# Kernel optimization log

Hardware: AMD Instinct MI355X
Metric: run time of the kernel (lower is better)

The kernel has to match this reference:

```python
import jax, jax.numpy as jnp
import numpy as np

N_USERS = 80000
N_ITEMS = 40000
N_NODES = N_USERS + N_ITEMS
EMBED_DIM = 128
N_LAYERS = 3
N_EDGES = 1600000
BATCH = 4096


def setup_inputs() -> dict:
    key = jax.random.key(0)
    k = jax.random.split(key, 7)
    # Xavier-uniform-ish embeddings
    bound_u = float(np.sqrt(6.0 / (N_USERS + EMBED_DIM)))
    bound_i = float(np.sqrt(6.0 / (N_ITEMS + EMBED_DIM)))
    user_emb = jax.random.uniform(k[0], (N_USERS, EMBED_DIM), jnp.float32, -bound_u, bound_u)
    item_emb = jax.random.uniform(k[1], (N_ITEMS, EMBED_DIM), jnp.float32, -bound_i, bound_i)
    edge_rows = jax.random.randint(k[2], (N_EDGES,), 0, N_NODES, dtype=jnp.int32)
    edge_cols = jax.random.randint(k[3], (N_EDGES,), 0, N_NODES, dtype=jnp.int32)
    # normalized adjacency values (positive, small) standing in for D^-1/2 A D^-1/2
    edge_vals = jax.random.uniform(k[4], (N_EDGES,), jnp.float32, 0.0, 0.1)
    users = jax.random.randint(k[5], (BATCH,), 0, N_USERS, dtype=jnp.int32)
    items = jax.random.randint(k[6], (BATCH,), 0, N_ITEMS, dtype=jnp.int32)
    return {"user_emb": user_emb, "item_emb": item_emb,
            "edge_rows": edge_rows, "edge_cols": edge_cols, "edge_vals": edge_vals,
            "users": users, "items": items}


def _spmm(edge_rows, edge_cols, edge_vals, x):
    # out[r] += vals[e] * x[cols[e]]  for each edge e with rows[e]==r
    msgs = edge_vals[:, None] * x[edge_cols]          # [E, D]
    return jax.ops.segment_sum(msgs, edge_rows, num_segments=N_NODES)


def reference(user_emb, item_emb, edge_rows, edge_cols, edge_vals, users, items):
    all_emb = jnp.concatenate([user_emb, item_emb], axis=0)  # [N, D]
    acc = all_emb
    x = all_emb
    for _ in range(N_LAYERS):
        x = _spmm(edge_rows, edge_cols, edge_vals, x)
        acc = acc + x
    final = acc / jnp.asarray(N_LAYERS + 1, dtype=acc.dtype)  # mean over stacked layers
    user_all, item_all = final[:N_USERS], final[N_USERS:]
    return user_all[users], item_all[items]
```

## Files before the change

### kernel.cpp

```cpp
#include <hip/hip_runtime.h>

#define N_USERS 80000
#define N_ITEMS 40000
#define N_NODES 120000
#define DIM 128
#define N_EDGES 1600000
#define BATCH 4096

#define RPB 512
#define NB  ((N_NODES + RPB - 1) / RPB)
#define BCAP 8192
#define CHUNK 2048
#define NCHUNK ((N_EDGES + CHUNK - 1) / CHUNK)

#define INITX_BLOCKS (N_NODES * 16 / 256)
#define GATHI_BLOCKS (2 * BATCH * 32 / 256)
#define SAMP_BLOCKS  (2 * BATCH / 256)
#define KSAMP 8

__device__ __forceinline__ float bf_lo(unsigned u) { return __uint_as_float(u << 16); }
__device__ __forceinline__ float bf_hi(unsigned u) { return __uint_as_float(u & 0xFFFF0000u); }
__device__ __forceinline__ unsigned pack_bf2(float a, float b) {
    unsigned ua = __float_as_uint(a);
    ua = (ua + 0x7FFFu + ((ua >> 16) & 1u)) >> 16;
    unsigned ub = __float_as_uint(b);
    ub = (ub + 0x7FFFu + ((ub >> 16) & 1u)) & 0xFFFF0000u;
    return ua | ub;
}

__global__ void partition_prep_kernel(const int* __restrict__ rows,
                                      const int* __restrict__ cols,
                                      const float* __restrict__ vals,
                                      const float* __restrict__ ue,
                                      const float* __restrict__ ie,
                                      const int* __restrict__ users,
                                      const int* __restrict__ items,
                                      int* __restrict__ bucket_cursor,
                                      int2* __restrict__ temp,
                                      uint4* __restrict__ xb,
                                      float4* __restrict__ out,
                                      int* __restrict__ scnt,
                                      int* __restrict__ sidx) {
    __shared__ int cnt[256];
    __shared__ int sc[256];
    __shared__ int loff[256];
    __shared__ int gbase[256];
    __shared__ int lcur[256];
    __shared__ int2 stage[CHUNK];
    __shared__ unsigned char sbkt[CHUNK];

    int tid = threadIdx.x;
    int bid = blockIdx.x;

    if (bid < NCHUNK) {
        int base = bid * CHUNK;
        int nloc = min(CHUNK, N_EDGES - base);

        cnt[tid] = 0;
        __syncthreads();

        int my_r[CHUNK / 256];
        int my_c[CHUNK / 256];
        float my_v[CHUNK / 256];
        for (int k = 0; k < CHUNK / 256; ++k) {
            int i = tid + k * 256;
            if (i < nloc) {
                int e = base + i;
                int r = rows[e];
                my_r[k] = r;
                my_c[k] = cols[e];
                my_v[k] = vals[e];
                atomicAdd(&cnt[r >> 9], 1);
            }
        }
        __syncthreads();

        sc[tid] = cnt[tid];
        __syncthreads();
        for (int off = 1; off < 256; off <<= 1) {
            int t = (tid >= off) ? sc[tid - off] : 0;
            __syncthreads();
            sc[tid] += t;
            __syncthreads();
        }
        loff[tid] = sc[tid] - cnt[tid];
        if (tid < NB && cnt[tid] > 0)
            gbase[tid] = tid * BCAP + atomicAdd(&bucket_cursor[tid], cnt[tid]);
        lcur[tid] = 0;
        __syncthreads();

        for (int k = 0; k < CHUNK / 256; ++k) {
            int i = tid + k * 256;
            if (i < nloc) {
                int b = my_r[k] >> 9;
                int rank = atomicAdd(&lcur[b], 1);
                int s = loff[b] + rank;
                stage[s] = make_int2(((my_r[k] & (RPB - 1)) << 17) | my_c[k],
                                     __float_as_int(my_v[k]));
                sbkt[s] = (unsigned char)b;
            }
        }
        __syncthreads();

        for (int k = 0; k < CHUNK / 256; ++k) {
            int s = tid + k * 256;
            if (s < nloc) {
                int b = sbkt[s];
                temp[gbase[b] + (s - loff[b])] = stage[s];
            }
        }
    } else if (bid < NCHUNK + INITX_BLOCKS) {
        int t = (bid - NCHUNK) * 256 + tid;
        int n = t >> 4;
        int c = t & 15;
        const float* src = (n < N_USERS) ? (ue + (size_t)n * DIM)
                                         : (ie + (size_t)(n - N_USERS) * DIM);
        float4 a = ((const float4*)src)[c * 2];
        float4 b = ((const float4*)src)[c * 2 + 1];
        uint4 o;
        o.x = pack_bf2(a.x, a.y);
        o.y = pack_bf2(a.z, a.w);
        o.z = pack_bf2(b.x, b.y);
        o.w = pack_bf2(b.z, b.w);
        xb[t] = o;
    } else if (bid < NCHUNK + INITX_BLOCKS + GATHI_BLOCKS) {
        int t = (bid - NCHUNK - INITX_BLOCKS) * 256 + tid;
        int half = t >> 17;
        int i = t & (BATCH * 32 - 1);
        int b = i >> 5;
        int c = i & 31;
        float4 v;
        if (half == 0) {
            int u = users[b];
            v = ((const float4*)(ue + (size_t)u * DIM))[c];
        } else {
            int it = items[b];
            v = ((const float4*)(ie + (size_t)it * DIM))[c];
        }
        out[t] = v;
    } else {
        int idx = (bid - NCHUNK - INITX_BLOCKS - GATHI_BLOCKS) * 256 + tid;
        if (idx < 2 * BATCH) {
            int node = (idx < BATCH) ? users[idx] : (N_USERS + items[idx - BATCH]);
            int slot = atomicAdd(&scnt[node], 1);
            if (slot < KSAMP) sidx[node * KSAMP + slot] = idx;
        }
    }
}

__global__ void bucket_sort_kernel(const int* __restrict__ bucket_cursor,
                                   const int2* __restrict__ temp,
                                   int2* __restrict__ ep,
                                   int* __restrict__ row_beg,
                                   int* __restrict__ row_end) {
    __shared__ int rcnt[RPB];
    __shared__ int rsc[RPB];
    __shared__ int rcur[RPB];
    int tid = threadIdx.x;
    int b = blockIdx.x;
    int beg = b * BCAP;
    int end = beg + bucket_cursor[b];

    if (tid < RPB) rcnt[tid] = 0;
    __syncthreads();
    for (int i = beg + tid; i < end; i += 1024) {
        int lr = temp[i].x >> 17;
        atomicAdd(&rcnt[lr], 1);
    }
    __syncthreads();

    int v = (tid < RPB) ? rcnt[tid] : 0;
    if (tid < RPB) rsc[tid] = v;
    __syncthreads();
    for (int off = 1; off < RPB; off <<= 1) {
        int t = (tid >= off && tid < RPB) ? rsc[tid - off] : 0;
        __syncthreads();
        if (tid < RPB) rsc[tid] += t;
        __syncthreads();
    }
    if (tid < RPB) {
        int excl = rsc[tid] - v;
        int row = (b << 9) + tid;
        if (row < N_NODES) {
            row_beg[row] = beg + excl;
            row_end[row] = beg + excl + v;
        }
        rcur[tid] = excl;
    }
    __syncthreads();

    for (int i = beg + tid; i < end; i += 1024) {
        int2 t = temp[i];
        int lr = t.x >> 17;
        int col = t.x & 0x1FFFF;
        int rank = atomicAdd(&rcur[lr], 1);
        ep[beg + rank] = make_int2(col, t.y);
    }
}

#define FMA8(V, M)                                                           \
    {                                                                        \
        acc[0] += (V) * bf_lo((M).x); acc[1] += (V) * bf_hi((M).x);          \
        acc[2] += (V) * bf_lo((M).y); acc[3] += (V) * bf_hi((M).y);          \
        acc[4] += (V) * bf_lo((M).z); acc[5] += (V) * bf_hi((M).z);          \
        acc[6] += (V) * bf_lo((M).w); acc[7] += (V) * bf_hi((M).w);          \
    }

#define ROW_ACC_LOOP(BEG, END)                                               \
    int j = (BEG);                                                           \
    for (; j + 8 <= (END); j += 8) {                                         \
        int2 e[8];                                                           \
        uint4 m[8];                                                          \
        _Pragma("unroll")                                                    \
        for (int k = 0; k < 8; ++k) e[k] = ep[j + k];                        \
        _Pragma("unroll")                                                    \
        for (int k = 0; k < 8; ++k) m[k] = xb[(size_t)e[k].x * 16 + c];      \
        _Pragma("unroll")                                                    \
        for (int k = 0; k < 8; ++k) {                                        \
            float v = __int_as_float(e[k].y);                                \
            FMA8(v, m[k]);                                                   \
        }                                                                    \
    }                                                                        \
    for (; j + 2 <= (END); j += 2) {                                         \
        int2 e0 = ep[j];                                                     \
        int2 e1 = ep[j + 1];                                                 \
        uint4 m0 = xb[(size_t)e0.x * 16 + c];                                \
        uint4 m1 = xb[(size_t)e1.x * 16 + c];                                \
        float v0 = __int_as_float(e0.y);                                     \
        float v1 = __int_as_float(e1.y);                                     \
        FMA8(v0, m0);                                                        \
        FMA8(v1, m1);                                                        \
    }                                                                        \
    if (j < (END)) {                                                         \
        int2 e0 = ep[j];                                                     \
        uint4 m0 = xb[(size_t)e0.x * 16 + c];                                \
        float v0 = __int_as_float(e0.y);                                     \
        FMA8(v0, m0);                                                        \
    }

__global__ void spmm_csr_bf16_kernel(const int* __restrict__ row_beg,
                                     const int* __restrict__ row_end,
                                     const int2* __restrict__ ep,
                                     const uint4* __restrict__ xb,
                                     uint4* __restrict__ yb,
                                     const int* __restrict__ scnt,
                                     const int* __restrict__ sidx,
                                     float4* __restrict__ out) {
    int t = blockIdx.x * blockDim.x + threadIdx.x;
    int r = t >> 4;
    int c = t & 15;
    if (r >= N_NODES) return;
    float acc[8] = {0.f, 0.f, 0.f, 0.f, 0.f, 0.f, 0.f, 0.f};
    { ROW_ACC_LOOP(row_beg[r], row_end[r]) }

    uint4 o;
    o.x = pack_bf2(acc[0], acc[1]);
    o.y = pack_bf2(acc[2], acc[3]);
    o.z = pack_bf2(acc[4], acc[5]);
    o.w = pack_bf2(acc[6], acc[7]);
    yb[(size_t)r * 16 + c] = o;

    int cnt = scnt[r];
    if (cnt > 0) {
        if (cnt > KSAMP) cnt = KSAMP;
        for (int k = 0; k < cnt; ++k) {
            int slot = sidx[r * KSAMP + k];
            float4* op = out + ((size_t)slot * 32 + c * 2);
            float4 o0 = op[0];
            float4 o1 = op[1];
            o0.x += acc[0]; o0.y += acc[1]; o0.z += acc[2]; o0.w += acc[3];
            o1.x += acc[4]; o1.y += acc[5]; o1.z += acc[6]; o1.w += acc[7];
            op[0] = o0;
            op[1] = o1;
        }
    }
}

__global__ void spmm_out_kernel(const int* __restrict__ row_beg,
                                const int* __restrict__ row_end,
                                const int2* __restrict__ ep,
                                const uint4* __restrict__ xb,
                                const int* __restrict__ users,
                                const int* __restrict__ items,
                                float4* __restrict__ out,
                                float scale) {
    int t = blockIdx.x * blockDim.x + threadIdx.x;
    int slot = t >> 4;
    int c = t & 15;
    if (slot >= 2 * BATCH) return;
    int r = (slot < BATCH) ? users[slot] : (N_USERS + items[slot - BATCH]);
    float acc[8] = {0.f, 0.f, 0.f, 0.f, 0.f, 0.f, 0.f, 0.f};
    { ROW_ACC_LOOP(row_beg[r], row_end[r]) }

    float4* op = out + ((size_t)slot * 32 + c * 2);
    float4 o0 = op[0];
    float4 o1 = op[1];
    o0.x = (o0.x + acc[0]) * scale;
    o0.y = (o0.y + acc[1]) * scale;
    o0.z = (o0.z + acc[2]) * scale;
    o0.w = (o0.w + acc[3]) * scale;
    o1.x = (o1.x + acc[4]) * scale;
    o1.y = (o1.y + acc[5]) * scale;
    o1.z = (o1.z + acc[6]) * scale;
    o1.w = (o1.w + acc[7]) * scale;
    op[0] = o0;
    op[1] = o1;
}

extern "C" void kernel_launch(void* const* d_in, const int* in_sizes, int n_in,
                              void* d_out, int out_size, void* d_ws, size_t ws_size,
                              hipStream_t stream) {
    const float* ue    = (const float*)d_in[0];
    const float* ie    = (const float*)d_in[1];
    const int*   rows  = (const int*)d_in[2];
    const int*   cols  = (const int*)d_in[3];
    const float* vals  = (const float*)d_in[4];
    const int*   users = (const int*)d_in[5];
    const int*   items = (const int*)d_in[6];
    float* out = (float*)d_out;

    int2*  ep    = (int2*)d_ws;
    int2*  temp  = ep + (size_t)NB * BCAP;
    uint4* xbuf0 = (uint4*)(temp + (size_t)NB * BCAP);
    uint4* xbuf1 = xbuf0 + (size_t)N_NODES * 16;
    int*   row_beg = (int*)(xbuf1 + (size_t)N_NODES * 16);
    int*   row_end = row_beg + N_NODES;
    int*   bucket_cursor = row_end + N_NODES;
    int*   scnt = bucket_cursor + NB;
    int*   sidx = scnt + N_NODES;

    uint4* xb = xbuf0;
    uint4* yb = xbuf1;

    hipMemsetAsync(bucket_cursor, 0, (NB + N_NODES) * sizeof(int), stream);

    partition_prep_kernel<<<NCHUNK + INITX_BLOCKS + GATHI_BLOCKS + SAMP_BLOCKS, 256, 0, stream>>>(
        rows, cols, vals, ue, ie, users, items,
        bucket_cursor, temp, xb, (float4*)out, scnt, sidx);

    bucket_sort_kernel<<<NB, 1024, 0, stream>>>(bucket_cursor, temp, ep, row_beg, row_end);

    for (int layer = 0; layer < 2; ++layer) {
        spmm_csr_bf16_kernel<<<(N_NODES * 16 + 255) / 256, 256, 0, stream>>>(
            row_beg, row_end, ep, xb, yb, scnt, sidx, (float4*)out);
        uint4* tmp = xb; xb = yb; yb = tmp;
    }
    spmm_out_kernel<<<(2 * BATCH * 16 + 255) / 256, 256, 0, stream>>>(
        row_beg, row_end, ep, xb, users, items, (float4*)out, 0.25f);
}
```

Before: 291.4 us.

## Fuse bucket sort with first SpMM layer using shared-memory sorted edges

Merges the per-bucket row sort with the first SpMM layer: each block sorts its bucket's edges into shared memory, writes them out as CSR, then computes layer one for its 256 rows straight from the shared-memory edge list. Buckets shrink to 256 rows (capacity 4096) and the partition kernel moves to 512-thread blocks. This removes one kernel launch and one global read of the edge list. In exchange it uses 32KB of shared memory per block and gives the SpMM phase only about 470 blocks with a serial 8-pass loop, which may hurt latency hiding.

```diff
diff --git a/kernel.cpp b/kernel.cpp
--- a/kernel.cpp
+++ b/kernel.cpp
@@ -7,15 +7,15 @@
 #define N_EDGES 1600000
 #define BATCH 4096
 
-#define RPB 512
+#define RPB 256
 #define NB  ((N_NODES + RPB - 1) / RPB)
-#define BCAP 8192
+#define BCAP 4096
 #define CHUNK 2048
 #define NCHUNK ((N_EDGES + CHUNK - 1) / CHUNK)
 
-#define INITX_BLOCKS (N_NODES * 16 / 256)
-#define GATHI_BLOCKS (2 * BATCH * 32 / 256)
-#define SAMP_BLOCKS  (2 * BATCH / 256)
+#define INITX_BLOCKS (N_NODES * 16 / 512)
+#define GATHI_BLOCKS (2 * BATCH * 32 / 512)
+#define SAMP_BLOCKS  (2 * BATCH / 512)
 #define KSAMP 8
 
 __device__ __forceinline__ float bf_lo(unsigned u) { return __uint_as_float(u << 16); }
@@ -28,26 +28,27 @@
     return ua | ub;
 }
 
-__global__ void partition_prep_kernel(const int* __restrict__ rows,
-                                      const int* __restrict__ cols,
-                                      const float* __restrict__ vals,
-                                      const float* __restrict__ ue,
-                                      const float* __restrict__ ie,
-                                      const int* __restrict__ users,
-                                      const int* __restrict__ items,
-                                      int* __restrict__ bucket_cursor,
-                                      int2* __restrict__ temp,
-                                      uint4* __restrict__ xb,
-                                      float4* __restrict__ out,
-                                      int* __restrict__ scnt,
-                                      int* __restrict__ sidx) {
-    __shared__ int cnt[256];
-    __shared__ int sc[256];
-    __shared__ int loff[256];
-    __shared__ int gbase[256];
-    __shared__ int lcur[256];
+__global__ __launch_bounds__(512) void partition_prep_kernel(
+        const int* __restrict__ rows,
+        const int* __restrict__ cols,
+        const float* __restrict__ vals,
+        const float* __restrict__ ue,
+        const float* __restrict__ ie,
+        const int* __restrict__ users,
+        const int* __restrict__ items,
+        int* __restrict__ bucket_cursor,
+        int2* __restrict__ temp,
+        uint4* __restrict__ xb,
+        float4* __restrict__ out,
+        int* __restrict__ scnt,
+        int* __restrict__ sidx) {
+    __shared__ int cnt[512];
+    __shared__ int sc[512];
+    __shared__ int loff[512];
+    __shared__ int gbase[512];
+    __shared__ int lcur[512];
     __shared__ int2 stage[CHUNK];
-    __shared__ unsigned char sbkt[CHUNK];
+    __shared__ unsigned short sbkt[CHUNK];
 
     int tid = threadIdx.x;
     int bid = blockIdx.x;
@@ -59,25 +60,26 @@
         cnt[tid] = 0;
         __syncthreads();
 
-        int my_r[CHUNK / 256];
-        int my_c[CHUNK / 256];
-        float my_v[CHUNK / 256];
-        for (int k = 0; k < CHUNK / 256; ++k) {
-            int i = tid + k * 256;
+        int my_r[CHUNK / 512];
+        int my_c[CHUNK / 512];
+        float my_v[CHUNK / 512];
+#pragma unroll
+        for (int k = 0; k < CHUNK / 512; ++k) {
+            int i = tid + k * 512;
             if (i < nloc) {
                 int e = base + i;
                 int r = rows[e];
                 my_r[k] = r;
                 my_c[k] = cols[e];
                 my_v[k] = vals[e];
-                atomicAdd(&cnt[r >> 9], 1);
+                atomicAdd(&cnt[r >> 8], 1);
             }
         }
         __syncthreads();
 
         sc[tid] = cnt[tid];
         __syncthreads();
-        for (int off = 1; off < 256; off <<= 1) {
+        for (int off = 1; off < 512; off <<= 1) {
             int t = (tid >= off) ? sc[tid - off] : 0;
             __syncthreads();
             sc[tid] += t;
@@ -89,28 +91,30 @@
         lcur[tid] = 0;
         __syncthreads();
 
-        for (int k = 0; k < CHUNK / 256; ++k) {
-            int i = tid + k * 256;
+#pragma unroll
+        for (int k = 0; k < CHUNK / 512; ++k) {
+            int i = tid + k * 512;
             if (i < nloc) {
-                int b = my_r[k] >> 9;
+                int b = my_r[k] >> 8;
                 int rank = atomicAdd(&lcur[b], 1);
                 int s = loff[b] + rank;
                 stage[s] = make_int2(((my_r[k] & (RPB - 1)) << 17) | my_c[k],
                                      __float_as_int(my_v[k]));
-                sbkt[s] = (unsigned char)b;
+                sbkt[s] = (unsigned short)b;
             }
         }
         __syncthreads();
 
-        for (int k = 0; k < CHUNK / 256; ++k) {
-            int s = tid + k * 256;
+#pragma unroll
+        for (int k = 0; k < CHUNK / 512; ++k) {
+            int s = tid + k * 512;
             if (s < nloc) {
                 int b = sbkt[s];
                 temp[gbase[b] + (s - loff[b])] = stage[s];
             }
         }
     } else if (bid < NCHUNK + INITX_BLOCKS) {
-        int t = (bid - NCHUNK) * 256 + tid;
+        int t = (bid - NCHUNK) * 512 + tid;
         int n = t >> 4;
         int c = t & 15;
         const float* src = (n < N_USERS) ? (ue + (size_t)n * DIM)
@@ -124,7 +128,7 @@
         o.w = pack_bf2(b.z, b.w);
         xb[t] = o;
     } else if (bid < NCHUNK + INITX_BLOCKS + GATHI_BLOCKS) {
-        int t = (bid - NCHUNK - INITX_BLOCKS) * 256 + tid;
+        int t = (bid - NCHUNK - INITX_BLOCKS) * 512 + tid;
         int half = t >> 17;
         int i = t & (BATCH * 32 - 1);
         int b = i >> 5;
@@ -139,62 +143,12 @@
         }
         out[t] = v;
     } else {
-        int idx = (bid - NCHUNK - INITX_BLOCKS - GATHI_BLOCKS) * 256 + tid;
+        int idx = (bid - NCHUNK - INITX_BLOCKS - GATHI_BLOCKS) * 512 + tid;
         if (idx < 2 * BATCH) {
             int node = (idx < BATCH) ? users[idx] : (N_USERS + items[idx - BATCH]);
             int slot = atomicAdd(&scnt[node], 1);
             if (slot < KSAMP) sidx[node * KSAMP + slot] = idx;
         }
-    }
-}
-
-__global__ void bucket_sort_kernel(const int* __restrict__ bucket_cursor,
-                                   const int2* __restrict__ temp,
-                                   int2* __restrict__ ep,
-                                   int* __restrict__ row_beg,
-                                   int* __restrict__ row_end) {
-    __shared__ int rcnt[RPB];
-    __shared__ int rsc[RPB];
-    __shared__ int rcur[RPB];
-    int tid = threadIdx.x;
-    int b = blockIdx.x;
-    int beg = b * BCAP;
-    int end = beg + bucket_cursor[b];
-
-    if (tid < RPB) rcnt[tid] = 0;
-    __syncthreads();
-    for (int i = beg + tid; i < end; i += 1024) {
-        int lr = temp[i].x >> 17;
-        atomicAdd(&rcnt[lr], 1);
-    }
-    __syncthreads();
-
-    int v = (tid < RPB) ? rcnt[tid] : 0;
-    if (tid < RPB) rsc[tid] = v;
-    __syncthreads();
-    for (int off = 1; off < RPB; off <<= 1) {
-        int t = (tid >= off && tid < RPB) ? rsc[tid - off] : 0;
-        __syncthreads();
-        if (tid < RPB) rsc[tid] += t;
-        __syncthreads();
-    }
-    if (tid < RPB) {
-        int excl = rsc[tid] - v;
-        int row = (b << 9) + tid;
-        if (row < N_NODES) {
-            row_beg[row] = beg + excl;
-            row_end[row] = beg + excl + v;
-        }
-        rcur[tid] = excl;
-    }
-    __syncthreads();
-
-    for (int i = beg + tid; i < end; i += 1024) {
-        int2 t = temp[i];
-        int lr = t.x >> 17;
-        int col = t.x & 0x1FFFF;
-        int rank = atomicAdd(&rcur[lr], 1);
-        ep[beg + rank] = make_int2(col, t.y);
     }
 }
 
@@ -206,13 +160,13 @@
         acc[6] += (V) * bf_lo((M).w); acc[7] += (V) * bf_hi((M).w);          \
     }
 
-#define ROW_ACC_LOOP(BEG, END)                                               \
+#define ROW_ACC_LOOP(EPTR, BEG, END)                                         \
     int j = (BEG);                                                           \
     for (; j + 8 <= (END); j += 8) {                                         \
         int2 e[8];                                                           \
         uint4 m[8];                                                          \
         _Pragma("unroll")                                                    \
-        for (int k = 0; k < 8; ++k) e[k] = ep[j + k];                        \
+        for (int k = 0; k < 8; ++k) e[k] = (EPTR)[j + k];                    \
         _Pragma("unroll")                                                    \
         for (int k = 0; k < 8; ++k) m[k] = xb[(size_t)e[k].x * 16 + c];      \
         _Pragma("unroll")                                                    \
@@ -222,8 +176,8 @@
         }                                                                    \
     }                                                                        \
     for (; j + 2 <= (END); j += 2) {                                         \
-        int2 e0 = ep[j];                                                     \
-        int2 e1 = ep[j + 1];                                                 \
+        int2 e0 = (EPTR)[j];                                                 \
+        int2 e1 = (EPTR)[j + 1];                                             \
         uint4 m0 = xb[(size_t)e0.x * 16 + c];                                \
         uint4 m1 = xb[(size_t)e1.x * 16 + c];                                \
         float v0 = __int_as_float(e0.y);                                     \
@@ -232,11 +186,121 @@
         FMA8(v1, m1);                                                        \
     }                                                                        \
     if (j < (END)) {                                                         \
-        int2 e0 = ep[j];                                                     \
+        int2 e0 = (EPTR)[j];                                                 \
         uint4 m0 = xb[(size_t)e0.x * 16 + c];                                \
         float v0 = __int_as_float(e0.y);                                     \
         FMA8(v0, m0);                                                        \
     }
+
+__global__ __launch_bounds__(512) void sort_spmm1_kernel(
+        const int* __restrict__ bucket_cursor,
+        const int2* __restrict__ temp,
+        int2* __restrict__ ep,
+        int* __restrict__ row_beg,
+        int* __restrict__ row_end,
+        const uint4* __restrict__ xb,
+        uint4* __restrict__ yb,
+        const int* __restrict__ scnt,
+        const int* __restrict__ sidx,
+        float4* __restrict__ out) {
+    __shared__ int rcnt[RPB];
+    __shared__ int rsc[RPB];
+    __shared__ int rcur[RPB];
+    __shared__ int2 srt[BCAP];
+
+    int tid = threadIdx.x;
+    int b = blockIdx.x;
+    int beg = b * BCAP;
+    int cnt = bucket_cursor[b];
+
+    if (tid < RPB) rcnt[tid] = 0;
+    __syncthreads();
+
+    int2 e[BCAP / 512];
+#pragma unroll
+    for (int k = 0; k < BCAP / 512; ++k) {
+        int idx = tid + k * 512;
+        if (idx < cnt) {
+            e[k] = temp[beg + idx];
+            atomicAdd(&rcnt[e[k].x >> 17], 1);
+        }
+    }
+    __syncthreads();
+
+    int v = 0;
+    if (tid < RPB) {
+        v = rcnt[tid];
+        rsc[tid] = v;
+    }
+    __syncthreads();
+    for (int off = 1; off < RPB; off <<= 1) {
+        int t = (tid < RPB && tid >= off) ? rsc[tid - off] : 0;
+        __syncthreads();
+        if (tid < RPB) rsc[tid] += t;
+        __syncthreads();
+    }
+    if (tid < RPB) {
+        int excl = rsc[tid] - v;
+        int row = (b << 8) + tid;
+        if (row < N_NODES) {
+            row_beg[row] = beg + excl;
+            row_end[row] = beg + rsc[tid];
+        }
+        rcur[tid] = excl;
+    }
+    __syncthreads();
+
+#pragma unroll
+    for (int k = 0; k < BCAP / 512; ++k) {
+        int idx = tid + k * 512;
+        if (idx < cnt) {
+            int lr = e[k].x >> 17;
+            int rank = atomicAdd(&rcur[lr], 1);
+            srt[rank] = make_int2(e[k].x & 0x1FFFF, e[k].y);
+        }
+    }
+    __syncthreads();
+
+#pragma unroll
+    for (int k = 0; k < BCAP / 512; ++k) {
+        int idx = tid + k * 512;
+        if (idx < cnt) ep[beg + idx] = srt[idx];
+    }
+
+    for (int g = 0; g < (RPB * 16) / 512; ++g) {
+        int u = g * 512 + tid;
+        int lr = u >> 4;
+        int c = u & 15;
+        int r = (b << 8) + lr;
+        if (r >= N_NODES) continue;
+        int jb = rsc[lr] - rcnt[lr];
+        int je = rsc[lr];
+        float acc[8] = {0.f, 0.f, 0.f, 0.f, 0.f, 0.f, 0.f, 0.f};
+        { ROW_ACC_LOOP(srt, jb, je) }
+
+        uint4 o;
+        o.x = pack_bf2(acc[0], acc[1]);
+        o.y = pack_bf2(acc[2], acc[3]);
+        o.z = pack_bf2(acc[4], acc[5]);
+        o.w = pack_bf2(acc[6], acc[7]);
+        yb[(size_t)r * 16 + c] = o;
+
+        int sn = scnt[r];
+        if (sn > 0) {
+            if (sn > KSAMP) sn = KSAMP;
+            for (int k = 0; k < sn; ++k) {
+                int slot = sidx[r * KSAMP + k];
+                float4* op = out + ((size_t)slot * 32 + c * 2);
+                float4 o0 = op[0];
+                float4 o1 = op[1];
+                o0.x += acc[0]; o0.y += acc[1]; o0.z += acc[2]; o0.w += acc[3];
+                o1.x += acc[4]; o1.y += acc[5]; o1.z += acc[6]; o1.w += acc[7];
+                op[0] = o0;
+                op[1] = o1;
+            }
+        }
+    }
+}
 
 __global__ void spmm_csr_bf16_kernel(const int* __restrict__ row_beg,
                                      const int* __restrict__ row_end,
@@ -251,7 +315,7 @@
     int c = t & 15;
     if (r >= N_NODES) return;
     float acc[8] = {0.f, 0.f, 0.f, 0.f, 0.f, 0.f, 0.f, 0.f};
-    { ROW_ACC_LOOP(row_beg[r], row_end[r]) }
+    { ROW_ACC_LOOP(ep, row_beg[r], row_end[r]) }
 
     uint4 o;
     o.x = pack_bf2(acc[0], acc[1]);
@@ -290,7 +354,7 @@
     if (slot >= 2 * BATCH) return;
     int r = (slot < BATCH) ? users[slot] : (N_USERS + items[slot - BATCH]);
     float acc[8] = {0.f, 0.f, 0.f, 0.f, 0.f, 0.f, 0.f, 0.f};
-    { ROW_ACC_LOOP(row_beg[r], row_end[r]) }
+    { ROW_ACC_LOOP(ep, row_beg[r], row_end[r]) }
 
     float4* op = out + ((size_t)slot * 32 + c * 2);
     float4 o0 = op[0];
@@ -334,17 +398,16 @@
 
     hipMemsetAsync(bucket_cursor, 0, (NB + N_NODES) * sizeof(int), stream);
 
-    partition_prep_kernel<<<NCHUNK + INITX_BLOCKS + GATHI_BLOCKS + SAMP_BLOCKS, 256, 0, stream>>>(
+    partition_prep_kernel<<<NCHUNK + INITX_BLOCKS + GATHI_BLOCKS + SAMP_BLOCKS, 512, 0, stream>>>(
         rows, cols, vals, ue, ie, users, items,
         bucket_cursor, temp, xb, (float4*)out, scnt, sidx);
 
-    bucket_sort_kernel<<<NB, 1024, 0, stream>>>(bucket_cursor, temp, ep, row_beg, row_end);
-
-    for (int layer = 0; layer < 2; ++layer) {
-        spmm_csr_bf16_kernel<<<(N_NODES * 16 + 255) / 256, 256, 0, stream>>>(
-            row_beg, row_end, ep, xb, yb, scnt, sidx, (float4*)out);
-        uint4* tmp = xb; xb = yb; yb = tmp;
-    }
+    sort_spmm1_kernel<<<NB, 512, 0, stream>>>(
+        bucket_cursor, temp, ep, row_beg, row_end, xb, yb, scnt, sidx, (float4*)out);
+
+    spmm_csr_bf16_kernel<<<(N_NODES * 16 + 255) / 256, 256, 0, stream>>>(
+        row_beg, row_end, ep, yb, xb, scnt, sidx, (float4*)out);
+
     spmm_out_kernel<<<(2 * BATCH * 16 + 255) / 256, 256, 0, stream>>>(
         row_beg, row_end, ep, xb, users, items, (float4*)out, 0.25f);
 }
```

New measurement: 277.9 us. -4.7%, faster.
